# Kernel optimization log

Measured on AMD Instinct MI355X. Metric: run time of the kernel, lower is better.

The kernel has to match this reference:

```python
import jax, jax.numpy as jnp
import numpy as np

N, L, S, E, A, D = 16, 256, 128, 128, 9, 768
ARG_ROLES = 23      # score width = ARG_ROLES + 1
MAX_ARG = 9         # hard-coded max_len_arg in the torch module
N_HID = 768


def setup_inputs() -> dict:
    key = jax.random.key(0)
    ks = jax.random.split(key, 10)
    all_embeddings = jax.random.normal(ks[0], (N, L, D), jnp.float32)
    # last-3-layer BERT attention maps, 12 heads, positive entries
    attn_last3 = jax.random.uniform(ks[1], (3, N, 12, L, L), jnp.float32)
    # per-sample sorted distinct first-subword indices (all positive, full length:
    # the ragged filter idxs>0 then keeps everything -> fixed-shape gather)
    idx_keys = jax.random.split(ks[2], N)
    cand = jnp.arange(1, L - MAX_ARG - 1)
    idxs_to_collect = jax.vmap(
        lambda k: jnp.sort(jax.random.choice(k, cand, (S + 2,), replace=False))
    )(idx_keys).astype(jnp.int32)
    is_triggers = (jax.random.uniform(ks[3], (N, S)) < 0.05).astype(jnp.float32)
    is_triggers = is_triggers.at[:, 0].set(1.0)  # >=1 trigger per sample
    entity_mapping = jax.random.normal(ks[4], (N, S, E), jnp.float32) * 0.05
    arg_weight_matrices = jax.random.normal(ks[5], (N, MAX_ARG, A), jnp.float32) * 0.3
    map_keys = jax.random.split(ks[6], N)
    arg_mapping = jax.vmap(
        lambda k: jax.random.permutation(k, ARG_ROLES + 1)[:A]
    )(map_keys).astype(jnp.int32)
    W1 = jax.random.normal(ks[7], (6 * D, N_HID), jnp.float32) * 0.02
    b1 = jnp.zeros((N_HID,), jnp.float32)
    W2 = jax.random.normal(ks[8], (N_HID, 1), jnp.float32) * 0.02
    b2 = jnp.zeros((1,), jnp.float32)
    return {
        "all_embeddings": all_embeddings,
        "attn_last3": attn_last3,
        "entity_mapping": entity_mapping,
        "arg_weight_matrices": arg_weight_matrices,
        "is_triggers": is_triggers,
        "W1": W1, "b1": b1, "W2": W2, "b2": b2,
        "idxs_to_collect": idxs_to_collect,
        "arg_mapping": arg_mapping,
    }


def reference(all_embeddings, attn_last3, entity_mapping, arg_weight_matrices,
              is_triggers, W1, b1, W2, b2, idxs_to_collect, arg_mapping):
    sqrt_d = jnp.sqrt(jnp.asarray(D, jnp.float32))
    sent_idx = idxs_to_collect[:, :S]                      # [N,S] first-subword ids
    # get_fist_subword_embeddings: ragged gather (full-length here)
    sent_emb = jnp.take_along_axis(all_embeddings, sent_idx[:, :, None], axis=1)  # [N,S,D]
    # arg-type tokens sit right after the second-to-last [SEP]
    arg_pos = idxs_to_collect[:, -2:-1] + 1 + jnp.arange(MAX_ARG)[None, :]        # [N,9]
    arg_raw = jnp.take_along_axis(all_embeddings, arg_pos[:, :, None], axis=1)    # [N,9,D]

    entity_emb = jnp.einsum('nsd,nse->ned', sent_emb, entity_mapping)             # [N,E,D]
    trig = jnp.sum(sent_emb * is_triggers[..., None], axis=1) \
           / jnp.sum(is_triggers, axis=1, keepdims=True)                          # [N,D]
    del trig  # _trigger is computed but unused downstream in the torch forward
    arg_emb = jnp.einsum('nkd,nka->nad', arg_raw, arg_weight_matrices)            # [N,A,D]

    # bi-attention scores (broadcast-mul-sum == contraction over D)
    t2a = jnp.einsum('ned,nad->nea', entity_emb, arg_emb) / sqrt_d
    w = (t2a - 5.0) / 2.0                                                         # [N,E,A]
    token_argAwared = jnp.einsum('nea,nad->ned', w, arg_emb)                      # [N,E,D]
    arg_tokenAwared = jnp.einsum('nea,ned->nad', w, entity_emb)                   # [N,A,D]

    # select_hidden_att for each of the last 3 layers
    att_mean = jnp.mean(attn_last3, axis=2)                                       # [3,N,L,L]
    def sel_layer(a):  # a: [N,L,L] -> row/col gather + row renorm
        s = jax.vmap(lambda m, i: m[i][:, i])(a, sent_idx)                        # [N,S,S]
        return s / (jnp.sum(s, axis=-1, keepdims=True) + 1e-9)
    t2t = (sel_layer(att_mean[0]) + sel_layer(att_mean[1]) + sel_layer(att_mean[2])) / 3.0

    h2h_sent = jnp.einsum('nst,ntd->nsd', t2t, sent_emb)                          # [N,S,D]
    # A_h2h and H_ are projected from sent space (S) to entity space (E)
    A_h2h_e = jnp.einsum('nsd,nse->ned', h2h_sent, entity_mapping)                # [N,E,D]
    H_e = entity_emb                                                              # sent_emb projected == entity_emb

    a2a = jax.nn.softmax(jnp.einsum('nad,nbd->nab', arg_emb, arg_emb), axis=-1)   # [N,A,A]
    u2u = jnp.einsum('nab,nbd->nad', a2a, arg_emb)                                # [N,A,D]

    shp = (N, E, A, D)
    H_    = jnp.broadcast_to(H_e[:, :, None, :], shp)
    U_    = jnp.broadcast_to(arg_emb[:, None, :, :], shp)
    A_h2u = jnp.broadcast_to(token_argAwared[:, :, None, :], shp)
    A_h2h = jnp.broadcast_to(A_h2h_e[:, :, None, :], shp)
    A_u2h = jnp.broadcast_to(arg_tokenAwared[:, None, :, :], shp)
    A_u2u = jnp.broadcast_to(u2u[:, None, :, :], shp)
    latent = jnp.concatenate([H_, U_, A_h2u, A_h2h, A_u2h, A_u2u], axis=-1)       # [N,E,A,6D]

    hid = jax.nn.gelu(latent @ W1 + b1, approximate=False)                        # [N,E,A,768]
    score = (hid @ W2 + b2)[..., 0]                                               # [N,E,A]

    # map_arg_to_ids: scatter each arg slot back to its global role id
    def scatter_one(s, ids):  # s [E,A], ids [A]
        return jnp.full((E, ARG_ROLES + 1), -1e6, jnp.float32).at[:, ids].set(s)
    new_score = jax.vmap(scatter_one)(score, arg_mapping)                         # [N,E,24]
    return new_score
```

## Files before the change

### kernel.cpp

```cpp
#include <hip/hip_runtime.h>
#include <math.h>

namespace {
constexpr int N_ = 16, L_ = 256, S_ = 128, E_ = 128, A_ = 9, D_ = 768, H_ = 768, RO_ = 24;
constexpr int IDXW = 130;
constexpr int W1R = 6 * D_;
constexpr float INV_SQRT_D = 0.03608439182435161f;
constexpr int PESZ = 2048 * 768;
constexpr int PASZ = 144 * 768;
constexpr int GB_GATHER = 0;
constexpr int GB_ENTMAP = 192;
constexpr int GB_W1T    = 208;
constexpr int GB_T2T    = 1072;
constexpr int GB_ARGU   = 2096;
constexpr int GB_TOTAL  = 2112;
}

using bshort8 = __attribute__((ext_vector_type(8))) short;
using f32x4v = __attribute__((ext_vector_type(4))) float;

__device__ __forceinline__ unsigned short f2bf(float f) {
    unsigned u = __builtin_bit_cast(unsigned, f);
    return (unsigned short)((u + 0x7fffu + ((u >> 16) & 1u)) >> 16);
}

__global__ __launch_bounds__(256) void stage1_k(const float* __restrict__ all_emb,
                                                const int* __restrict__ idxs,
                                                const float* __restrict__ ent_map,
                                                const float* __restrict__ W1,
                                                const float* __restrict__ argw,
                                                const float* __restrict__ attn,
                                                unsigned short* __restrict__ sentT,
                                                unsigned short* __restrict__ entmapT,
                                                short* __restrict__ W1t,
                                                unsigned short* __restrict__ t2tbf,
                                                float* __restrict__ argE,
                                                unsigned short* __restrict__ argEbf,
                                                unsigned short* __restrict__ u2ubf) {
    __shared__ __align__(16) unsigned char smem[33792];
    const int b = blockIdx.x, tid = threadIdx.x;

    if (b < GB_ENTMAP) {
        const int n = b / 12, d0 = (b % 12) * 64;
        auto tile = (unsigned short (*)[132])smem;
#pragma unroll
        for (int it = 0; it < 8; ++it) {
            const int lin = tid + 256 * it;
            const int s = lin >> 4, dq = (lin & 15) * 4;
            const int row = idxs[n * IDXW + s];
            const float4 v = *reinterpret_cast<const float4*>(all_emb + ((size_t)(n * L_ + row)) * D_ + d0 + dq);
            tile[dq + 0][s] = f2bf(v.x); tile[dq + 1][s] = f2bf(v.y);
            tile[dq + 2][s] = f2bf(v.z); tile[dq + 3][s] = f2bf(v.w);
        }
        __syncthreads();
#pragma unroll
        for (int it = 0; it < 8; ++it) {
            const int lin = tid + 256 * it;
            const int d = lin >> 5, s4 = (lin & 31) * 4;
            ushort4 v = {tile[d][s4], tile[d][s4 + 1], tile[d][s4 + 2], tile[d][s4 + 3]};
            *reinterpret_cast<ushort4*>(sentT + ((size_t)(n * D_) + d0 + d) * S_ + s4) = v;
        }
    } else if (b < GB_W1T) {
        const int n = b - GB_ENTMAP;
        auto tile = (unsigned short (*)[132])smem;
#pragma unroll
        for (int it = 0; it < 16; ++it) {
            const int lin = tid + 256 * it;
            const int s = lin >> 5, eq = (lin & 31) * 4;
            const float4 v = *reinterpret_cast<const float4*>(ent_map + ((size_t)(n * S_ + s)) * E_ + eq);
            tile[eq + 0][s] = f2bf(v.x); tile[eq + 1][s] = f2bf(v.y);
            tile[eq + 2][s] = f2bf(v.z); tile[eq + 3][s] = f2bf(v.w);
        }
        __syncthreads();
#pragma unroll
        for (int it = 0; it < 16; ++it) {
            const int lin = tid + 256 * it;
            const int e = lin >> 5, s4 = (lin & 31) * 4;
            ushort4 v = {tile[e][s4], tile[e][s4 + 1], tile[e][s4 + 2], tile[e][s4 + 3]};
            *reinterpret_cast<ushort4*>(entmapT + ((size_t)(n * E_) + e) * S_ + s4) = v;
        }
    } else if (b < GB_T2T) {
        const int b2 = b - GB_W1T;
        const int k0 = (b2 % 72) * 64, h0 = (b2 / 72) * 64;
        auto tile = (float (*)[65])smem;
        const int tx = tid & 63, ty = tid >> 6;
#pragma unroll
        for (int i = 0; i < 16; ++i) {
            const int r = ty + i * 4;
            tile[r][tx] = W1[(size_t)(k0 + r) * H_ + h0 + tx];
        }
        __syncthreads();
#pragma unroll
        for (int i = 0; i < 16; ++i) {
            const int r = ty + i * 4;
            W1t[(size_t)(h0 + r) * W1R + k0 + tx] = (short)f2bf(tile[tx][r]);
        }
    } else if (b < GB_ARGU) {
        const int idx = b - GB_T2T;
        const int n = idx >> 6;
        const int half = tid >> 7, t128 = tid & 127;
        const int s = ((idx & 63) << 1) | half;
        const int w = t128 >> 6, lane = tid & 63;
        float* sum2 = (float*)smem;
        float* part = (float*)(smem + 12288);
        const int is = idxs[n * IDXW + s], it = idxs[n * IDXW + t128];
#pragma unroll
        for (int l = 0; l < 3; ++l) {
            const float* base = attn + ((size_t)((l * N_ + n) * 12 + w * 6)) * (L_ * L_)
                              + (size_t)is * L_ + lane * 4;
            float4 acc = {0.f, 0.f, 0.f, 0.f};
#pragma unroll
            for (int h = 0; h < 6; ++h) {
                const float4 v = *reinterpret_cast<const float4*>(base + (size_t)h * (L_ * L_));
                acc.x += v.x; acc.y += v.y; acc.z += v.z; acc.w += v.w;
            }
            *reinterpret_cast<float4*>(&sum2[(((half * 3 + l) * 2 + w) << 8) + lane * 4]) = acc;
        }
        __syncthreads();
        float m[3];
#pragma unroll
        for (int l = 0; l < 3; ++l) {
            m[l] = (sum2[(((half * 3 + l) * 2 + 0) << 8) + it] +
                    sum2[(((half * 3 + l) * 2 + 1) << 8) + it]) * (1.0f / 12.0f);
            float r = m[l];
#pragma unroll
            for (int off = 32; off; off >>= 1) r += __shfl_xor(r, off, 64);
            if (lane == 0) part[(half * 3 + l) * 2 + w] = r;
        }
        __syncthreads();
        float out = 0.f;
#pragma unroll
        for (int l = 0; l < 3; ++l)
            out += m[l] / (part[(half * 3 + l) * 2 + 0] + part[(half * 3 + l) * 2 + 1] + 1e-9f);
        t2tbf[((size_t)(n * S_ + s)) * S_ + t128] = f2bf(out * (1.0f / 3.0f));
    } else {
        const int n = b - GB_ARGU;
        auto wsm = (float (*)[A_])smem;
        auto part45 = (float (*)[4])(smem + 512);
        auto Psm = (float (*)[A_])(smem + 1536);
        if (tid < A_ * A_) wsm[tid / A_][tid % A_] = argw[n * A_ * A_ + tid];
        __syncthreads();
        const int p0 = idxs[n * IDXW + S_] + 1;
        float pp[45] = {};
        float vals[3][A_];
#pragma unroll
        for (int c = 0; c < 3; ++c) {
            const int d = tid + 256 * c;
            float raw[A_];
#pragma unroll
            for (int k = 0; k < A_; ++k) raw[k] = all_emb[((size_t)(n * L_ + p0 + k)) * D_ + d];
#pragma unroll
            for (int a = 0; a < A_; ++a) {
                float acc = 0.f;
#pragma unroll
                for (int k = 0; k < A_; ++k) acc = fmaf(raw[k], wsm[k][a], acc);
                vals[c][a] = acc;
                argE[((size_t)(n * A_ + a)) * D_ + d] = acc;
                argEbf[((size_t)(n * A_ + a)) * D_ + d] = f2bf(acc);
            }
            int p = 0;
#pragma unroll
            for (int a = 0; a < A_; ++a)
#pragma unroll
                for (int bb = a; bb < A_; ++bb) pp[p++] += vals[c][a] * vals[c][bb];
        }
        const int lane = tid & 63, wv = tid >> 6;
#pragma unroll
        for (int p = 0; p < 45; ++p) {
            float v = pp[p];
            for (int off = 32; off; off >>= 1) v += __shfl_down(v, off, 64);
            if (lane == 0) part45[p][wv] = v;
        }
        __syncthreads();
        if (tid < 45) part45[tid][0] = part45[tid][0] + part45[tid][1] + part45[tid][2] + part45[tid][3];
        __syncthreads();
        if (tid < A_) {
            const int a = tid;
            float v[A_], mx = -1e30f;
#pragma unroll
            for (int bb = 0; bb < A_; ++bb) {
                const int lo = a < bb ? a : bb, hi = a < bb ? bb : a;
                v[bb] = part45[lo * (19 - lo) / 2 + hi - lo][0];
                mx = fmaxf(mx, v[bb]);
            }
            float sm = 0.f;
#pragma unroll
            for (int bb = 0; bb < A_; ++bb) { v[bb] = expf(v[bb] - mx); sm += v[bb]; }
            const float inv = 1.0f / sm;
#pragma unroll
            for (int bb = 0; bb < A_; ++bb) Psm[a][bb] = v[bb] * inv;
        }
        __syncthreads();
#pragma unroll
        for (int c = 0; c < 3; ++c) {
            const int d = tid + 256 * c;
#pragma unroll
            for (int a = 0; a < A_; ++a) {
                float acc = 0.f;
#pragma unroll
                for (int bb = 0; bb < A_; ++bb) acc = fmaf(Psm[a][bb], vals[c][bb], acc);
                u2ubf[((size_t)(n * A_ + a)) * D_ + d] = f2bf(acc);
            }
        }
    }
}

__global__ __launch_bounds__(256) void gemm_pair_k(const unsigned short* __restrict__ t2tbf,
                                                   const unsigned short* __restrict__ entmapT,
                                                   const unsigned short* __restrict__ sentT,
                                                   float* __restrict__ entf,
                                                   unsigned short* __restrict__ entbf,
                                                   unsigned short* __restrict__ h2hT) {
    __shared__ __align__(16) short As[128][40];
    __shared__ __align__(16) short Bs[64][40];
    const int n = blockIdx.y, c0 = blockIdx.x * 64, z = blockIdx.z;
    const unsigned short* A = (z == 0 ? t2tbf : entmapT) + (size_t)n * S_ * S_;
    const unsigned short* BT = sentT + (size_t)n * D_ * S_;
    const int tid = threadIdx.x;
    const int wave = tid >> 6, lane = tid & 63;
    const int row16 = lane & 15, quad = lane >> 4;
    f32x4v acc[2][4] = {};
    for (int k0 = 0; k0 < S_; k0 += 32) {
#pragma unroll
        for (int i = 0; i < 2; ++i) {
            const int idx = tid + 256 * i;
            const int r = idx >> 2, q = idx & 3;
            *reinterpret_cast<bshort8*>(&As[r][q * 8]) =
                *reinterpret_cast<const bshort8*>(A + (size_t)r * S_ + k0 + q * 8);
        }
        {
            const int col = tid >> 2, q = tid & 3;
            *reinterpret_cast<bshort8*>(&Bs[col][q * 8]) =
                *reinterpret_cast<const bshort8*>(BT + (size_t)(c0 + col) * S_ + k0 + q * 8);
        }
        __syncthreads();
        bshort8 a[2], b[4];
#pragma unroll
        for (int mi = 0; mi < 2; ++mi)
            a[mi] = *reinterpret_cast<const bshort8*>(&As[wave * 32 + mi * 16 + row16][quad * 8]);
#pragma unroll
        for (int ni = 0; ni < 4; ++ni)
            b[ni] = *reinterpret_cast<const bshort8*>(&Bs[ni * 16 + row16][quad * 8]);
#pragma unroll
        for (int mi = 0; mi < 2; ++mi)
#pragma unroll
            for (int ni = 0; ni < 4; ++ni)
                acc[mi][ni] = __builtin_amdgcn_mfma_f32_16x16x32_bf16(a[mi], b[ni], acc[mi][ni], 0, 0, 0);
        __syncthreads();
    }
#pragma unroll
    for (int mi = 0; mi < 2; ++mi) {
#pragma unroll
        for (int ni = 0; ni < 4; ++ni) {
            const int rbase = wave * 32 + mi * 16 + quad * 4;
            const int col = c0 + ni * 16 + row16;
            if (z == 0) {
                ushort4 v = {f2bf(acc[mi][ni][0]), f2bf(acc[mi][ni][1]),
                             f2bf(acc[mi][ni][2]), f2bf(acc[mi][ni][3])};
                *reinterpret_cast<ushort4*>(h2hT + (size_t)n * D_ * S_ + (size_t)col * S_ + rbase) = v;
            } else {
#pragma unroll
                for (int t = 0; t < 4; ++t) {
                    const size_t o = ((size_t)n * S_ + rbase + t) * D_ + col;
                    entf[o] = acc[mi][ni][t];
                    entbf[o] = f2bf(acc[mi][ni][t]);
                }
            }
        }
    }
}

__global__ __launch_bounds__(256) void gemm2_k(const unsigned short* __restrict__ entmapT,
                                               const unsigned short* __restrict__ h2hT,
                                               const unsigned short* __restrict__ entbf,
                                               const unsigned short* __restrict__ argEbf,
                                               unsigned short* __restrict__ Ah2hbf,
                                               float* __restrict__ wbuf) {
    const int bx = blockIdx.x, tid = threadIdx.x;
    const int wave = tid >> 6, lane = tid & 63;
    const int row16 = lane & 15, quad = lane >> 4;
    if (bx < 192) {
        __shared__ __align__(16) short As[128][40];
        __shared__ __align__(16) short Bs[64][40];
        const int n = bx / 12, c0 = (bx % 12) * 64;
        const unsigned short* A = entmapT + (size_t)n * S_ * S_;
        const unsigned short* BT = h2hT + (size_t)n * D_ * S_;
        f32x4v acc[2][4] = {};
        for (int k0 = 0; k0 < S_; k0 += 32) {
#pragma unroll
            for (int i = 0; i < 2; ++i) {
                const int idx = tid + 256 * i;
                const int r = idx >> 2, q = idx & 3;
                *reinterpret_cast<bshort8*>(&As[r][q * 8]) =
                    *reinterpret_cast<const bshort8*>(A + (size_t)r * S_ + k0 + q * 8);
            }
            {
                const int col = tid >> 2, q = tid & 3;
                *reinterpret_cast<bshort8*>(&Bs[col][q * 8]) =
                    *reinterpret_cast<const bshort8*>(BT + (size_t)(c0 + col) * S_ + k0 + q * 8);
            }
            __syncthreads();
            bshort8 a[2], b[4];
#pragma unroll
            for (int mi = 0; mi < 2; ++mi)
                a[mi] = *reinterpret_cast<const bshort8*>(&As[wave * 32 + mi * 16 + row16][quad * 8]);
#pragma unroll
            for (int ni = 0; ni < 4; ++ni)
                b[ni] = *reinterpret_cast<const bshort8*>(&Bs[ni * 16 + row16][quad * 8]);
#pragma unroll
            for (int mi = 0; mi < 2; ++mi)
#pragma unroll
                for (int ni = 0; ni < 4; ++ni)
                    acc[mi][ni] = __builtin_amdgcn_mfma_f32_16x16x32_bf16(a[mi], b[ni], acc[mi][ni], 0, 0, 0);
            __syncthreads();
        }
#pragma unroll
        for (int mi = 0; mi < 2; ++mi)
#pragma unroll
            for (int ni = 0; ni < 4; ++ni) {
                const int rbase = wave * 32 + mi * 16 + quad * 4;
                const int col = c0 + ni * 16 + row16;
#pragma unroll
                for (int t = 0; t < 4; ++t)
                    Ah2hbf[((size_t)n * S_ + rbase + t) * D_ + col] = f2bf(acc[mi][ni][t]);
            }
    } else {
        const int n = bx - 192;
        const unsigned short* Aent = entbf + (size_t)n * E_ * D_;
        const unsigned short* Barg = argEbf + (size_t)n * A_ * D_;
        f32x4v acc[2] = {};
        for (int k0 = 0; k0 < D_; k0 += 32) {
            bshort8 a[2], b;
#pragma unroll
            for (int mi = 0; mi < 2; ++mi)
                a[mi] = *reinterpret_cast<const bshort8*>(Aent + (size_t)(wave * 32 + mi * 16 + row16) * D_ + k0 + quad * 8);
            b = *reinterpret_cast<const bshort8*>(Barg + (size_t)row16 * D_ + k0 + quad * 8);
#pragma unroll
            for (int mi = 0; mi < 2; ++mi)
                acc[mi] = __builtin_amdgcn_mfma_f32_16x16x32_bf16(a[mi], b, acc[mi], 0, 0, 0);
        }
        if (row16 < A_) {
#pragma unroll
            for (int mi = 0; mi < 2; ++mi)
#pragma unroll
                for (int t = 0; t < 4; ++t) {
                    const int e = wave * 32 + mi * 16 + quad * 4 + t;
                    const float w = (acc[mi][t] * INV_SQRT_D - 5.0f) * 0.5f;
                    wbuf[((size_t)(n * E_ + e)) * A_ + row16] = w;
                }
        }
    }
}

__global__ __launch_bounds__(256) void post_k(const float* __restrict__ wbuf,
                                              const float* __restrict__ argE,
                                              const float* __restrict__ entf,
                                              unsigned short* __restrict__ tokAbf,
                                              unsigned short* __restrict__ argTbf) {
    const int b = blockIdx.x, tid = threadIdx.x;
    if (b < N_ * E_) {
        const int n = b >> 7, e = b & 127;
        __shared__ float wl[A_];
        if (tid < A_) wl[tid] = wbuf[(size_t)(n * E_ + e) * A_ + tid];
        __syncthreads();
        const float* ar = argE + (size_t)n * A_ * D_;
#pragma unroll
        for (int c = 0; c < 3; ++c) {
            const int d = tid + 256 * c;
            float s = 0.f;
#pragma unroll
            for (int a = 0; a < A_; ++a) s = fmaf(wl[a], ar[(size_t)a * D_ + d], s);
            tokAbf[((size_t)(n * E_ + e)) * D_ + d] = f2bf(s);
        }
    } else {
        const int idx = b - N_ * E_;
        const int n = idx / A_, a = idx % A_;
        __shared__ float wl[E_];
        if (tid < E_) wl[tid] = wbuf[(size_t)(n * E_ + tid) * A_ + a];
        __syncthreads();
        const float* eb = entf + (size_t)n * E_ * D_;
#pragma unroll
        for (int c = 0; c < 3; ++c) {
            const int d = tid + 256 * c;
            float acc = 0.f;
            for (int e = 0; e < E_; ++e) acc = fmaf(wl[e], eb[(size_t)e * D_ + d], acc);
            argTbf[((size_t)(n * A_ + a)) * D_ + d] = f2bf(acc);
        }
    }
}

__global__ __launch_bounds__(256) void mfma_mlp_k(const unsigned short* __restrict__ e0,
                                                  const unsigned short* __restrict__ e1,
                                                  const unsigned short* __restrict__ e2,
                                                  const unsigned short* __restrict__ a0,
                                                  const unsigned short* __restrict__ a1,
                                                  const unsigned short* __restrict__ a2,
                                                  const short* __restrict__ W1t,
                                                  float* __restrict__ Pe3, float* __restrict__ Pa3) {
    __shared__ __align__(16) short As[128][40];
    __shared__ __align__(16) short Bs[64][40];
    const int bx = blockIdx.x;
    const int seg = bx % 3;
    const int blk = bx / 3;
    const bool isPa = blk >= 16;
    const unsigned short* Aseg;
    int woff;
    if (isPa) {
        Aseg = seg == 0 ? a0 : (seg == 1 ? a1 : a2);
        woff = seg == 0 ? 1 * D_ : (seg == 1 ? 4 * D_ : 5 * D_);
    } else {
        Aseg = seg == 0 ? e0 : (seg == 1 ? e1 : e2);
        woff = seg == 0 ? 0 : (seg == 1 ? 2 * D_ : 3 * D_);
    }
    const int M = isPa ? N_ * A_ : N_ * E_;
    const int r0 = (isPa ? blk - 16 : blk) * 128;
    float* C = isPa ? (Pa3 + (size_t)seg * PASZ) : (Pe3 + (size_t)seg * PESZ);
    const int c0 = blockIdx.y * 64;
    const int tid = threadIdx.x;
    const int wave = tid >> 6, lane = tid & 63;
    const int row16 = lane & 15, quad = lane >> 4;
    f32x4v acc[2][4] = {};
    for (int kk = 0; kk < D_; kk += 32) {
#pragma unroll
        for (int i = 0; i < 2; ++i) {
            const int idx = tid + 256 * i;
            const int r = idx >> 2, q = idx & 3;
            bshort8 av = {};
            if (r0 + r < M) av = *reinterpret_cast<const bshort8*>(Aseg + (size_t)(r0 + r) * D_ + kk + q * 8);
            *reinterpret_cast<bshort8*>(&As[r][q * 8]) = av;
        }
        {
            const int col = tid >> 2, q = tid & 3;
            *reinterpret_cast<bshort8*>(&Bs[col][q * 8]) =
                *reinterpret_cast<const bshort8*>(W1t + (size_t)(c0 + col) * W1R + woff + kk + q * 8);
        }
        __syncthreads();
        bshort8 a[2], b[4];
#pragma unroll
        for (int mi = 0; mi < 2; ++mi)
            a[mi] = *reinterpret_cast<const bshort8*>(&As[wave * 32 + mi * 16 + row16][quad * 8]);
#pragma unroll
        for (int ni = 0; ni < 4; ++ni)
            b[ni] = *reinterpret_cast<const bshort8*>(&Bs[ni * 16 + row16][quad * 8]);
#pragma unroll
        for (int mi = 0; mi < 2; ++mi)
#pragma unroll
            for (int ni = 0; ni < 4; ++ni)
                acc[mi][ni] = __builtin_amdgcn_mfma_f32_16x16x32_bf16(a[mi], b[ni], acc[mi][ni], 0, 0, 0);
        __syncthreads();
    }
#pragma unroll
    for (int mi = 0; mi < 2; ++mi) {
#pragma unroll
        for (int ni = 0; ni < 4; ++ni) {
            const int rbase = r0 + wave * 32 + mi * 16 + quad * 4;
            const int col = c0 + ni * 16 + row16;
#pragma unroll
            for (int t = 0; t < 4; ++t)
                if (rbase + t < M) C[(size_t)(rbase + t) * H_ + col] = acc[mi][ni][t];
        }
    }
}

__global__ __launch_bounds__(256) void score_k(const float* __restrict__ Pe3, const float* __restrict__ Pa3,
                                               const float* __restrict__ b1, const float* __restrict__ W2,
                                               const float* __restrict__ b2, const int* __restrict__ arg_map,
                                               float* __restrict__ out) {
    const int n = blockIdx.x >> 7, e = blockIdx.x & 127;
    const int tid = threadIdx.x;
    __shared__ float paS[A_ * H_];
    __shared__ float part[A_][4];
    float* orow = out + ((size_t)(n * E_ + e)) * RO_;
    if (tid < RO_) orow[tid] = -1000000.0f;
    for (int i = tid; i < A_ * H_; i += 256) {
        const size_t o = (size_t)n * A_ * H_ + i;
        paS[i] = Pa3[o] + Pa3[PASZ + o] + Pa3[2 * PASZ + o];
    }
    __syncthreads();
    const size_t ro = ((size_t)(n * E_ + e)) * H_;
    float acc[A_] = {};
    for (int h = tid; h < H_; h += 256) {
        const float pe = Pe3[ro + h] + Pe3[PESZ + ro + h] + Pe3[2 * PESZ + ro + h] + b1[h];
        const float w2 = W2[h];
#pragma unroll
        for (int a = 0; a < A_; ++a) {
            const float x = pe + paS[a * H_ + h];
            const float g = x * 0.5f * (1.0f + erff(x * 0.70710678118654752f));
            acc[a] = fmaf(g, w2, acc[a]);
        }
    }
    const int lane = tid & 63, wv = tid >> 6;
#pragma unroll
    for (int a = 0; a < A_; ++a)
        for (int off = 32; off; off >>= 1) acc[a] += __shfl_down(acc[a], off, 64);
    if (lane == 0)
        for (int a = 0; a < A_; ++a) part[a][wv] = acc[a];
    __syncthreads();
    if (tid < A_) {
        const float s = part[tid][0] + part[tid][1] + part[tid][2] + part[tid][3] + b2[0];
        orow[arg_map[n * A_ + tid]] = s;
    }
}

extern "C" void kernel_launch(void* const* d_in, const int* in_sizes, int n_in,
                              void* d_out, int out_size, void* d_ws, size_t ws_size,
                              hipStream_t stream) {
    const float* all_emb = (const float*)d_in[0];
    const float* attn    = (const float*)d_in[1];
    const float* ent_map = (const float*)d_in[2];
    const float* argw    = (const float*)d_in[3];
    const float* W1 = (const float*)d_in[5];
    const float* b1 = (const float*)d_in[6];
    const float* W2 = (const float*)d_in[7];
    const float* b2 = (const float*)d_in[8];
    const int* idxs    = (const int*)d_in[9];
    const int* arg_map = (const int*)d_in[10];
    float* out = (float*)d_out;

    float* ws = (float*)d_ws;
    float* entf = ws + 0;
    float* Pe3  = ws + 1572864;
    float* argE = ws + 6291456;
    float* wbuf = ws + 6402048;
    float* Pa3  = ws + 6420480;
    short*          W1t     = (short*)(ws + 6752256);
    unsigned short* sentT   = (unsigned short*)(ws + 8521728);
    unsigned short* entmapT = (unsigned short*)(ws + 9308160);
    unsigned short* t2tbf   = (unsigned short*)(ws + 9439232);
    unsigned short* argEbf  = (unsigned short*)(ws + 9570304);
    unsigned short* u2ubf   = (unsigned short*)(ws + 9625600);
    unsigned short* entbf   = (unsigned short*)(ws + 9680896);
    unsigned short* h2hT    = (unsigned short*)(ws + 10467328);
    unsigned short* Ah2hbf  = (unsigned short*)(ws + 11253760);
    unsigned short* tokAbf  = (unsigned short*)(ws + 12040192);
    unsigned short* argTbf  = (unsigned short*)(ws + 12826624);

    stage1_k<<<GB_TOTAL, 256, 0, stream>>>(all_emb, idxs, ent_map, W1, argw, attn,
                                           sentT, entmapT, W1t, t2tbf, argE, argEbf, u2ubf);

    gemm_pair_k<<<dim3(D_ / 64, N_, 2), 256, 0, stream>>>(t2tbf, entmapT, sentT, entf, entbf, h2hT);

    gemm2_k<<<208, 256, 0, stream>>>(entmapT, h2hT, entbf, argEbf, Ah2hbf, wbuf);

    post_k<<<N_ * E_ + N_ * A_, 256, 0, stream>>>(wbuf, argE, entf, tokAbf, argTbf);

    mfma_mlp_k<<<dim3(54, H_ / 64), 256, 0, stream>>>(entbf, tokAbf, Ah2hbf, argEbf, argTbf, u2ubf, W1t, Pe3, Pa3);

    score_k<<<N_ * E_, 256, 0, stream>>>(Pe3, Pa3, b1, W2, b2, arg_map, out);

    (void)in_sizes; (void)n_in; (void)out_size; (void)ws_size;
}
```

Before: 318.2 us.

## Reassociate A_h2h chain via entmap·t2t product and fuse post-GEMM stages

Instead of computing h2h = t2t·sent and then entmap·h2h over D columns, the code first forms the small S×S product entmap·t2t and then multiplies it by the sentence embeddings. This cuts the 768-wide intermediate GEMM. The gemm2/post kernels are merged into a single fused kernel that also computes the entity-arg weights in place with fp32 dot products, which drops one launch and the wbuf round-trip. It also reorders stage1 block ranges so the heavy t2t blocks go first, and swaps the MLP grid axes so column tiles vary fastest. The reassociation changes bf16 rounding order, and the fp32 dot-product loops may be slower per block.

Result: slower. 329.7 us (+3.6%).

```diff
diff --git a/kernel.cpp b/kernel.cpp
--- a/kernel.cpp
+++ b/kernel.cpp
@@ -8,10 +8,10 @@
 constexpr float INV_SQRT_D = 0.03608439182435161f;
 constexpr int PESZ = 2048 * 768;
 constexpr int PASZ = 144 * 768;
-constexpr int GB_GATHER = 0;
-constexpr int GB_ENTMAP = 192;
-constexpr int GB_W1T    = 208;
-constexpr int GB_T2T    = 1072;
+constexpr int GB_T2T    = 0;
+constexpr int GB_W1T    = 1024;
+constexpr int GB_GATHER = 1888;
+constexpr int GB_ENTMAP = 2080;
 constexpr int GB_ARGU   = 2096;
 constexpr int GB_TOTAL  = 2112;
 }
@@ -22,6 +22,43 @@
 __device__ __forceinline__ unsigned short f2bf(float f) {
     unsigned u = __builtin_bit_cast(unsigned, f);
     return (unsigned short)((u + 0x7fffu + ((u >> 16) & 1u)) >> 16);
+}
+
+__device__ __forceinline__ void gemm_body128(const unsigned short* __restrict__ A,
+                                             const unsigned short* __restrict__ BT,
+                                             int lda, int ldb, int c0, int tid,
+                                             short (*As)[40], short (*Bs)[40],
+                                             f32x4v acc[2][4]) {
+    const int wave = tid >> 6, lane = tid & 63;
+    const int row16 = lane & 15, quad = lane >> 4;
+    for (int k0 = 0; k0 < S_; k0 += 32) {
+#pragma unroll
+        for (int i = 0; i < 2; ++i) {
+            const int idx = tid + 256 * i;
+            const int r = idx >> 2, q = idx & 3;
+            *reinterpret_cast<bshort8*>(&As[r][q * 8]) =
+                *reinterpret_cast<const bshort8*>(A + (size_t)r * lda + k0 + q * 8);
+        }
+        {
+            const int col = tid >> 2, q = tid & 3;
+            *reinterpret_cast<bshort8*>(&Bs[col][q * 8]) =
+                *reinterpret_cast<const bshort8*>(BT + (size_t)(c0 + col) * ldb + k0 + q * 8);
+        }
+        __syncthreads();
+        bshort8 a[2], b[4];
+#pragma unroll
+        for (int mi = 0; mi < 2; ++mi)
+            a[mi] = *reinterpret_cast<const bshort8*>(&As[wave * 32 + mi * 16 + row16][quad * 8]);
+#pragma unroll
+        for (int ni = 0; ni < 4; ++ni)
+            b[ni] = *reinterpret_cast<const bshort8*>(&Bs[ni * 16 + row16][quad * 8]);
+#pragma unroll
+        for (int mi = 0; mi < 2; ++mi)
+#pragma unroll
+            for (int ni = 0; ni < 4; ++ni)
+                acc[mi][ni] = __builtin_amdgcn_mfma_f32_16x16x32_bf16(a[mi], b[ni], acc[mi][ni], 0, 0, 0);
+        __syncthreads();
+    }
 }
 
 __global__ __launch_bounds__(256) void stage1_k(const float* __restrict__ all_emb,
@@ -33,15 +70,77 @@
                                                 unsigned short* __restrict__ sentT,
                                                 unsigned short* __restrict__ entmapT,
                                                 short* __restrict__ W1t,
-                                                unsigned short* __restrict__ t2tbf,
+                                                unsigned short* __restrict__ t2tT,
                                                 float* __restrict__ argE,
                                                 unsigned short* __restrict__ argEbf,
                                                 unsigned short* __restrict__ u2ubf) {
     __shared__ __align__(16) unsigned char smem[33792];
     const int b = blockIdx.x, tid = threadIdx.x;
 
-    if (b < GB_ENTMAP) {
-        const int n = b / 12, d0 = (b % 12) * 64;
+    if (b < GB_W1T) {
+        const int idx = b - GB_T2T;
+        const int n = idx >> 6;
+        const int half = tid >> 7, t128 = tid & 127;
+        const int s0 = (idx & 63) << 1;
+        const int s = s0 | half;
+        const int w = t128 >> 6, lane = tid & 63;
+        float* sum2 = (float*)smem;
+        float* part = (float*)(smem + 12288);
+        unsigned short* tileT = (unsigned short*)(smem + 12544);
+        const int is = idxs[n * IDXW + s], it = idxs[n * IDXW + t128];
+#pragma unroll
+        for (int l = 0; l < 3; ++l) {
+            const float* base = attn + ((size_t)((l * N_ + n) * 12 + w * 6)) * (L_ * L_)
+                              + (size_t)is * L_ + lane * 4;
+            float4 acc = {0.f, 0.f, 0.f, 0.f};
+#pragma unroll
+            for (int h = 0; h < 6; ++h) {
+                const float4 v = *reinterpret_cast<const float4*>(base + (size_t)h * (L_ * L_));
+                acc.x += v.x; acc.y += v.y; acc.z += v.z; acc.w += v.w;
+            }
+            *reinterpret_cast<float4*>(&sum2[(((half * 3 + l) * 2 + w) << 8) + lane * 4]) = acc;
+        }
+        __syncthreads();
+        float m[3];
+#pragma unroll
+        for (int l = 0; l < 3; ++l) {
+            m[l] = (sum2[(((half * 3 + l) * 2 + 0) << 8) + it] +
+                    sum2[(((half * 3 + l) * 2 + 1) << 8) + it]) * (1.0f / 12.0f);
+            float r = m[l];
+#pragma unroll
+            for (int off = 32; off; off >>= 1) r += __shfl_xor(r, off, 64);
+            if (lane == 0) part[(half * 3 + l) * 2 + w] = r;
+        }
+        __syncthreads();
+        float out = 0.f;
+#pragma unroll
+        for (int l = 0; l < 3; ++l)
+            out += m[l] / (part[(half * 3 + l) * 2 + 0] + part[(half * 3 + l) * 2 + 1] + 1e-9f);
+        tileT[t128 * 2 + half] = f2bf(out * (1.0f / 3.0f));
+        __syncthreads();
+        if (tid < 128) {
+            const unsigned int v = ((const unsigned int*)tileT)[tid];
+            *reinterpret_cast<unsigned int*>(t2tT + ((size_t)(n * S_) + tid) * S_ + s0) = v;
+        }
+    } else if (b < GB_GATHER) {
+        const int b2 = b - GB_W1T;
+        const int k0 = (b2 % 72) * 64, h0 = (b2 / 72) * 64;
+        auto tile = (float (*)[65])smem;
+        const int tx = tid & 63, ty = tid >> 6;
+#pragma unroll
+        for (int i = 0; i < 16; ++i) {
+            const int r = ty + i * 4;
+            tile[r][tx] = W1[(size_t)(k0 + r) * H_ + h0 + tx];
+        }
+        __syncthreads();
+#pragma unroll
+        for (int i = 0; i < 16; ++i) {
+            const int r = ty + i * 4;
+            W1t[(size_t)(h0 + r) * W1R + k0 + tx] = (short)f2bf(tile[tx][r]);
+        }
+    } else if (b < GB_ENTMAP) {
+        const int b2 = b - GB_GATHER;
+        const int n = b2 / 12, d0 = (b2 % 12) * 64;
         auto tile = (unsigned short (*)[132])smem;
 #pragma unroll
         for (int it = 0; it < 8; ++it) {
@@ -60,7 +159,7 @@
             ushort4 v = {tile[d][s4], tile[d][s4 + 1], tile[d][s4 + 2], tile[d][s4 + 3]};
             *reinterpret_cast<ushort4*>(sentT + ((size_t)(n * D_) + d0 + d) * S_ + s4) = v;
         }
-    } else if (b < GB_W1T) {
+    } else if (b < GB_ARGU) {
         const int n = b - GB_ENTMAP;
         auto tile = (unsigned short (*)[132])smem;
 #pragma unroll
@@ -79,60 +178,6 @@
             ushort4 v = {tile[e][s4], tile[e][s4 + 1], tile[e][s4 + 2], tile[e][s4 + 3]};
             *reinterpret_cast<ushort4*>(entmapT + ((size_t)(n * E_) + e) * S_ + s4) = v;
         }
-    } else if (b < GB_T2T) {
-        const int b2 = b - GB_W1T;
-        const int k0 = (b2 % 72) * 64, h0 = (b2 / 72) * 64;
-        auto tile = (float (*)[65])smem;
-        const int tx = tid & 63, ty = tid >> 6;
-#pragma unroll
-        for (int i = 0; i < 16; ++i) {
-            const int r = ty + i * 4;
-            tile[r][tx] = W1[(size_t)(k0 + r) * H_ + h0 + tx];
-        }
-        __syncthreads();
-#pragma unroll
-        for (int i = 0; i < 16; ++i) {
-            const int r = ty + i * 4;
-            W1t[(size_t)(h0 + r) * W1R + k0 + tx] = (short)f2bf(tile[tx][r]);
-        }
-    } else if (b < GB_ARGU) {
-        const int idx = b - GB_T2T;
-        const int n = idx >> 6;
-        const int half = tid >> 7, t128 = tid & 127;
-        const int s = ((idx & 63) << 1) | half;
-        const int w = t128 >> 6, lane = tid & 63;
-        float* sum2 = (float*)smem;
-        float* part = (float*)(smem + 12288);
-        const int is = idxs[n * IDXW + s], it = idxs[n * IDXW + t128];
-#pragma unroll
-        for (int l = 0; l < 3; ++l) {
-            const float* base = attn + ((size_t)((l * N_ + n) * 12 + w * 6)) * (L_ * L_)
-                              + (size_t)is * L_ + lane * 4;
-            float4 acc = {0.f, 0.f, 0.f, 0.f};
-#pragma unroll
-            for (int h = 0; h < 6; ++h) {
-                const float4 v = *reinterpret_cast<const float4*>(base + (size_t)h * (L_ * L_));
-                acc.x += v.x; acc.y += v.y; acc.z += v.z; acc.w += v.w;
-            }
-            *reinterpret_cast<float4*>(&sum2[(((half * 3 + l) * 2 + w) << 8) + lane * 4]) = acc;
-        }
-        __syncthreads();
-        float m[3];
-#pragma unroll
-        for (int l = 0; l < 3; ++l) {
-            m[l] = (sum2[(((half * 3 + l) * 2 + 0) << 8) + it] +
-                    sum2[(((half * 3 + l) * 2 + 1) << 8) + it]) * (1.0f / 12.0f);
-            float r = m[l];
-#pragma unroll
-            for (int off = 32; off; off >>= 1) r += __shfl_xor(r, off, 64);
-            if (lane == 0) part[(half * 3 + l) * 2 + w] = r;
-        }
-        __syncthreads();
-        float out = 0.f;
-#pragma unroll
-        for (int l = 0; l < 3; ++l)
-            out += m[l] / (part[(half * 3 + l) * 2 + 0] + part[(half * 3 + l) * 2 + 1] + 1e-9f);
-        t2tbf[((size_t)(n * S_ + s)) * S_ + t128] = f2bf(out * (1.0f / 3.0f));
     } else {
         const int n = b - GB_ARGU;
         auto wsm = (float (*)[A_])smem;
@@ -205,115 +250,40 @@
     }
 }
 
-__global__ __launch_bounds__(256) void gemm_pair_k(const unsigned short* __restrict__ t2tbf,
-                                                   const unsigned short* __restrict__ entmapT,
-                                                   const unsigned short* __restrict__ sentT,
-                                                   float* __restrict__ entf,
-                                                   unsigned short* __restrict__ entbf,
-                                                   unsigned short* __restrict__ h2hT) {
+__global__ __launch_bounds__(256) void gemm_entM1_k(const unsigned short* __restrict__ entmapT,
+                                                    const unsigned short* __restrict__ sentT,
+                                                    const unsigned short* __restrict__ t2tT,
+                                                    float* __restrict__ entf,
+                                                    unsigned short* __restrict__ entbf,
+                                                    unsigned short* __restrict__ M1bf) {
     __shared__ __align__(16) short As[128][40];
     __shared__ __align__(16) short Bs[64][40];
-    const int n = blockIdx.y, c0 = blockIdx.x * 64, z = blockIdx.z;
-    const unsigned short* A = (z == 0 ? t2tbf : entmapT) + (size_t)n * S_ * S_;
-    const unsigned short* BT = sentT + (size_t)n * D_ * S_;
-    const int tid = threadIdx.x;
+    const int bx = blockIdx.x, tid = threadIdx.x;
     const int wave = tid >> 6, lane = tid & 63;
     const int row16 = lane & 15, quad = lane >> 4;
     f32x4v acc[2][4] = {};
-    for (int k0 = 0; k0 < S_; k0 += 32) {
-#pragma unroll
-        for (int i = 0; i < 2; ++i) {
-            const int idx = tid + 256 * i;
-            const int r = idx >> 2, q = idx & 3;
-            *reinterpret_cast<bshort8*>(&As[r][q * 8]) =
-                *reinterpret_cast<const bshort8*>(A + (size_t)r * S_ + k0 + q * 8);
-        }
-        {
-            const int col = tid >> 2, q = tid & 3;
-            *reinterpret_cast<bshort8*>(&Bs[col][q * 8]) =
-                *reinterpret_cast<const bshort8*>(BT + (size_t)(c0 + col) * S_ + k0 + q * 8);
-        }
-        __syncthreads();
-        bshort8 a[2], b[4];
-#pragma unroll
-        for (int mi = 0; mi < 2; ++mi)
-            a[mi] = *reinterpret_cast<const bshort8*>(&As[wave * 32 + mi * 16 + row16][quad * 8]);
-#pragma unroll
-        for (int ni = 0; ni < 4; ++ni)
-            b[ni] = *reinterpret_cast<const bshort8*>(&Bs[ni * 16 + row16][quad * 8]);
-#pragma unroll
-        for (int mi = 0; mi < 2; ++mi)
-#pragma unroll
-            for (int ni = 0; ni < 4; ++ni)
-                acc[mi][ni] = __builtin_amdgcn_mfma_f32_16x16x32_bf16(a[mi], b[ni], acc[mi][ni], 0, 0, 0);
-        __syncthreads();
-    }
-#pragma unroll
-    for (int mi = 0; mi < 2; ++mi) {
-#pragma unroll
-        for (int ni = 0; ni < 4; ++ni) {
-            const int rbase = wave * 32 + mi * 16 + quad * 4;
-            const int col = c0 + ni * 16 + row16;
-            if (z == 0) {
-                ushort4 v = {f2bf(acc[mi][ni][0]), f2bf(acc[mi][ni][1]),
-                             f2bf(acc[mi][ni][2]), f2bf(acc[mi][ni][3])};
-                *reinterpret_cast<ushort4*>(h2hT + (size_t)n * D_ * S_ + (size_t)col * S_ + rbase) = v;
-            } else {
+    if (bx < 192) {
+        const int n = bx / 12, c0 = (bx % 12) * 64;
+        gemm_body128(entmapT + (size_t)n * S_ * S_, sentT + (size_t)n * D_ * S_,
+                     S_, S_, c0, tid, As, Bs, acc);
+#pragma unroll
+        for (int mi = 0; mi < 2; ++mi)
+#pragma unroll
+            for (int ni = 0; ni < 4; ++ni) {
+                const int rbase = wave * 32 + mi * 16 + quad * 4;
+                const int col = c0 + ni * 16 + row16;
 #pragma unroll
                 for (int t = 0; t < 4; ++t) {
-                    const size_t o = ((size_t)n * S_ + rbase + t) * D_ + col;
+                    const size_t o = ((size_t)(n * S_) + rbase + t) * D_ + col;
                     entf[o] = acc[mi][ni][t];
                     entbf[o] = f2bf(acc[mi][ni][t]);
                 }
             }
-        }
-    }
-}
-
-__global__ __launch_bounds__(256) void gemm2_k(const unsigned short* __restrict__ entmapT,
-                                               const unsigned short* __restrict__ h2hT,
-                                               const unsigned short* __restrict__ entbf,
-                                               const unsigned short* __restrict__ argEbf,
-                                               unsigned short* __restrict__ Ah2hbf,
-                                               float* __restrict__ wbuf) {
-    const int bx = blockIdx.x, tid = threadIdx.x;
-    const int wave = tid >> 6, lane = tid & 63;
-    const int row16 = lane & 15, quad = lane >> 4;
-    if (bx < 192) {
-        __shared__ __align__(16) short As[128][40];
-        __shared__ __align__(16) short Bs[64][40];
-        const int n = bx / 12, c0 = (bx % 12) * 64;
-        const unsigned short* A = entmapT + (size_t)n * S_ * S_;
-        const unsigned short* BT = h2hT + (size_t)n * D_ * S_;
-        f32x4v acc[2][4] = {};
-        for (int k0 = 0; k0 < S_; k0 += 32) {
-#pragma unroll
-            for (int i = 0; i < 2; ++i) {
-                const int idx = tid + 256 * i;
-                const int r = idx >> 2, q = idx & 3;
-                *reinterpret_cast<bshort8*>(&As[r][q * 8]) =
-                    *reinterpret_cast<const bshort8*>(A + (size_t)r * S_ + k0 + q * 8);
-            }
-            {
-                const int col = tid >> 2, q = tid & 3;
-                *reinterpret_cast<bshort8*>(&Bs[col][q * 8]) =
-                    *reinterpret_cast<const bshort8*>(BT + (size_t)(c0 + col) * S_ + k0 + q * 8);
-            }
-            __syncthreads();
-            bshort8 a[2], b[4];
-#pragma unroll
-            for (int mi = 0; mi < 2; ++mi)
-                a[mi] = *reinterpret_cast<const bshort8*>(&As[wave * 32 + mi * 16 + row16][quad * 8]);
-#pragma unroll
-            for (int ni = 0; ni < 4; ++ni)
-                b[ni] = *reinterpret_cast<const bshort8*>(&Bs[ni * 16 + row16][quad * 8]);
-#pragma unroll
-            for (int mi = 0; mi < 2; ++mi)
-#pragma unroll
-                for (int ni = 0; ni < 4; ++ni)
-                    acc[mi][ni] = __builtin_amdgcn_mfma_f32_16x16x32_bf16(a[mi], b[ni], acc[mi][ni], 0, 0, 0);
-            __syncthreads();
-        }
+    } else {
+        const int idx = bx - 192;
+        const int n = idx >> 1, c0 = (idx & 1) * 64;
+        gemm_body128(entmapT + (size_t)n * S_ * S_, t2tT + (size_t)n * S_ * S_,
+                     S_, S_, c0, tid, As, Bs, acc);
 #pragma unroll
         for (int mi = 0; mi < 2; ++mi)
 #pragma unroll
@@ -322,61 +292,34 @@
                 const int col = c0 + ni * 16 + row16;
 #pragma unroll
                 for (int t = 0; t < 4; ++t)
-                    Ah2hbf[((size_t)n * S_ + rbase + t) * D_ + col] = f2bf(acc[mi][ni][t]);
-            }
-    } else {
-        const int n = bx - 192;
-        const unsigned short* Aent = entbf + (size_t)n * E_ * D_;
-        const unsigned short* Barg = argEbf + (size_t)n * A_ * D_;
-        f32x4v acc[2] = {};
-        for (int k0 = 0; k0 < D_; k0 += 32) {
-            bshort8 a[2], b;
-#pragma unroll
-            for (int mi = 0; mi < 2; ++mi)
-                a[mi] = *reinterpret_cast<const bshort8*>(Aent + (size_t)(wave * 32 + mi * 16 + row16) * D_ + k0 + quad * 8);
-            b = *reinterpret_cast<const bshort8*>(Barg + (size_t)row16 * D_ + k0 + quad * 8);
-#pragma unroll
-            for (int mi = 0; mi < 2; ++mi)
-                acc[mi] = __builtin_amdgcn_mfma_f32_16x16x32_bf16(a[mi], b, acc[mi], 0, 0, 0);
-        }
-        if (row16 < A_) {
-#pragma unroll
-            for (int mi = 0; mi < 2; ++mi)
-#pragma unroll
-                for (int t = 0; t < 4; ++t) {
-                    const int e = wave * 32 + mi * 16 + quad * 4 + t;
-                    const float w = (acc[mi][t] * INV_SQRT_D - 5.0f) * 0.5f;
-                    wbuf[((size_t)(n * E_ + e)) * A_ + row16] = w;
-                }
-        }
-    }
-}
-
-__global__ __launch_bounds__(256) void post_k(const float* __restrict__ wbuf,
-                                              const float* __restrict__ argE,
-                                              const float* __restrict__ entf,
-                                              unsigned short* __restrict__ tokAbf,
-                                              unsigned short* __restrict__ argTbf) {
-    const int b = blockIdx.x, tid = threadIdx.x;
-    if (b < N_ * E_) {
-        const int n = b >> 7, e = b & 127;
-        __shared__ float wl[A_];
-        if (tid < A_) wl[tid] = wbuf[(size_t)(n * E_ + e) * A_ + tid];
-        __syncthreads();
-        const float* ar = argE + (size_t)n * A_ * D_;
-#pragma unroll
-        for (int c = 0; c < 3; ++c) {
-            const int d = tid + 256 * c;
-            float s = 0.f;
-#pragma unroll
-            for (int a = 0; a < A_; ++a) s = fmaf(wl[a], ar[(size_t)a * D_ + d], s);
-            tokAbf[((size_t)(n * E_ + e)) * D_ + d] = f2bf(s);
-        }
-    } else {
-        const int idx = b - N_ * E_;
-        const int n = idx / A_, a = idx % A_;
-        __shared__ float wl[E_];
-        if (tid < E_) wl[tid] = wbuf[(size_t)(n * E_ + tid) * A_ + a];
+                    M1bf[((size_t)(n * S_) + rbase + t) * S_ + col] = f2bf(acc[mi][ni][t]);
+            }
+    }
+}
+
+__global__ __launch_bounds__(256) void fused3_k(const unsigned short* __restrict__ M1bf,
+                                                const unsigned short* __restrict__ sentT,
+                                                const float* __restrict__ entf,
+                                                const float* __restrict__ argE,
+                                                unsigned short* __restrict__ Ah2hbf,
+                                                unsigned short* __restrict__ tokAbf,
+                                                unsigned short* __restrict__ argTbf) {
+    __shared__ __align__(16) unsigned char smem[15872];
+    const int bx = blockIdx.x, tid = threadIdx.x;
+    if (bx < N_ * A_) {
+        const int n = bx / A_, a = bx % A_;
+        float* argS = (float*)smem;
+        float* wl = (float*)(smem + 3072);
+        for (int i = tid; i < D_; i += 256) argS[i] = argE[((size_t)(n * A_ + a)) * D_ + i];
+        __syncthreads();
+        {
+            const int e = tid >> 1, h = tid & 1;
+            const float* er = entf + ((size_t)(n * E_ + e)) * D_ + h * 384;
+            float p = 0.f;
+            for (int d = 0; d < 384; ++d) p = fmaf(er[d], argS[h * 384 + d], p);
+            p += __shfl_down(p, 1, 64);
+            if (h == 0) wl[e] = (p * INV_SQRT_D - 5.0f) * 0.5f;
+        }
         __syncthreads();
         const float* eb = entf + (size_t)n * E_ * D_;
 #pragma unroll
@@ -385,6 +328,58 @@
             float acc = 0.f;
             for (int e = 0; e < E_; ++e) acc = fmaf(wl[e], eb[(size_t)e * D_ + d], acc);
             argTbf[((size_t)(n * A_ + a)) * D_ + d] = f2bf(acc);
+        }
+    } else if (bx < N_ * A_ + 192) {
+        const int idx = bx - N_ * A_;
+        const int n = idx / 12, c0 = (idx % 12) * 64;
+        short (*As)[40] = (short (*)[40])smem;
+        short (*Bs)[40] = (short (*)[40])(smem + 10240);
+        const int wave = tid >> 6, lane = tid & 63;
+        const int row16 = lane & 15, quad = lane >> 4;
+        f32x4v acc[2][4] = {};
+        gemm_body128(M1bf + (size_t)n * S_ * S_, sentT + (size_t)n * D_ * S_,
+                     S_, S_, c0, tid, As, Bs, acc);
+#pragma unroll
+        for (int mi = 0; mi < 2; ++mi)
+#pragma unroll
+            for (int ni = 0; ni < 4; ++ni) {
+                const int rbase = wave * 32 + mi * 16 + quad * 4;
+                const int col = c0 + ni * 16 + row16;
+#pragma unroll
+                for (int t = 0; t < 4; ++t)
+                    Ah2hbf[((size_t)(n * S_) + rbase + t) * D_ + col] = f2bf(acc[mi][ni][t]);
+            }
+    } else {
+        const int idx = bx - (N_ * A_ + 192);
+        const int n = idx >> 7, e = idx & 127;
+        float* wl = (float*)smem;
+        float* part = (float*)(smem + 64);
+        const float* er = entf + ((size_t)(n * E_ + e)) * D_;
+        const float* ar = argE + (size_t)n * A_ * D_;
+        float acc[A_] = {};
+        for (int d = tid; d < D_; d += 256) {
+            const float ev = er[d];
+#pragma unroll
+            for (int a = 0; a < A_; ++a) acc[a] = fmaf(ev, ar[(size_t)a * D_ + d], acc[a]);
+        }
+        const int lane = tid & 63, wv = tid >> 6;
+#pragma unroll
+        for (int a = 0; a < A_; ++a)
+            for (int off = 32; off; off >>= 1) acc[a] += __shfl_down(acc[a], off, 64);
+        if (lane == 0)
+            for (int a = 0; a < A_; ++a) part[a * 4 + wv] = acc[a];
+        __syncthreads();
+        if (tid < A_)
+            wl[tid] = ((part[tid * 4] + part[tid * 4 + 1] + part[tid * 4 + 2] + part[tid * 4 + 3])
+                       * INV_SQRT_D - 5.0f) * 0.5f;
+        __syncthreads();
+#pragma unroll
+        for (int c = 0; c < 3; ++c) {
+            const int d = tid + 256 * c;
+            float s = 0.f;
+#pragma unroll
+            for (int a = 0; a < A_; ++a) s = fmaf(wl[a], ar[(size_t)a * D_ + d], s);
+            tokAbf[((size_t)(n * E_ + e)) * D_ + d] = f2bf(s);
         }
     }
 }
@@ -399,9 +394,10 @@
                                                   float* __restrict__ Pe3, float* __restrict__ Pa3) {
     __shared__ __align__(16) short As[128][40];
     __shared__ __align__(16) short Bs[64][40];
-    const int bx = blockIdx.x;
-    const int seg = bx % 3;
-    const int blk = bx / 3;
+    const int c0 = blockIdx.x * 64;
+    const int by = blockIdx.y;
+    const int seg = by / 18;
+    const int blk = by % 18;
     const bool isPa = blk >= 16;
     const unsigned short* Aseg;
     int woff;
@@ -415,7 +411,6 @@
     const int M = isPa ? N_ * A_ : N_ * E_;
     const int r0 = (isPa ? blk - 16 : blk) * 128;
     float* C = isPa ? (Pa3 + (size_t)seg * PASZ) : (Pe3 + (size_t)seg * PESZ);
-    const int c0 = blockIdx.y * 64;
     const int tid = threadIdx.x;
     const int wave = tid >> 6, lane = tid & 63;
     const int row16 = lane & 15, quad = lane >> 4;
@@ -521,30 +516,28 @@
     float* entf = ws + 0;
     float* Pe3  = ws + 1572864;
     float* argE = ws + 6291456;
-    float* wbuf = ws + 6402048;
-    float* Pa3  = ws + 6420480;
-    short*          W1t     = (short*)(ws + 6752256);
-    unsigned short* sentT   = (unsigned short*)(ws + 8521728);
-    unsigned short* entmapT = (unsigned short*)(ws + 9308160);
-    unsigned short* t2tbf   = (unsigned short*)(ws + 9439232);
-    unsigned short* argEbf  = (unsigned short*)(ws + 9570304);
-    unsigned short* u2ubf   = (unsigned short*)(ws + 9625600);
-    unsigned short* entbf   = (unsigned short*)(ws + 9680896);
-    unsigned short* h2hT    = (unsigned short*)(ws + 10467328);
-    unsigned short* Ah2hbf  = (unsigned short*)(ws + 11253760);
-    unsigned short* tokAbf  = (unsigned short*)(ws + 12040192);
-    unsigned short* argTbf  = (unsigned short*)(ws + 12826624);
+    float* Pa3  = ws + 6402048;
+    short*          W1t     = (short*)(ws + 6733824);
+    unsigned short* sentT   = (unsigned short*)(ws + 8503296);
+    unsigned short* entmapT = (unsigned short*)(ws + 9289728);
+    unsigned short* t2tT    = (unsigned short*)(ws + 9420800);
+    unsigned short* M1bf    = (unsigned short*)(ws + 9551872);
+    unsigned short* argEbf  = (unsigned short*)(ws + 9682944);
+    unsigned short* u2ubf   = (unsigned short*)(ws + 9738240);
+    unsigned short* entbf   = (unsigned short*)(ws + 9793536);
+    unsigned short* Ah2hbf  = (unsigned short*)(ws + 10579968);
+    unsigned short* tokAbf  = (unsigned short*)(ws + 11366400);
+    unsigned short* argTbf  = (unsigned short*)(ws + 12152832);
 
     stage1_k<<<GB_TOTAL, 256, 0, stream>>>(all_emb, idxs, ent_map, W1, argw, attn,
-                                           sentT, entmapT, W1t, t2tbf, argE, argEbf, u2ubf);
-
-    gemm_pair_k<<<dim3(D_ / 64, N_, 2), 256, 0, stream>>>(t2tbf, entmapT, sentT, entf, entbf, h2hT);
-
-    gemm2_k<<<208, 256, 0, stream>>>(entmapT, h2hT, entbf, argEbf, Ah2hbf, wbuf);
-
-    post_k<<<N_ * E_ + N_ * A_, 256, 0, stream>>>(wbuf, argE, entf, tokAbf, argTbf);
-
-    mfma_mlp_k<<<dim3(54, H_ / 64), 256, 0, stream>>>(entbf, tokAbf, Ah2hbf, argEbf, argTbf, u2ubf, W1t, Pe3, Pa3);
+                                           sentT, entmapT, W1t, t2tT, argE, argEbf, u2ubf);
+
+    gemm_entM1_k<<<224, 256, 0, stream>>>(entmapT, sentT, t2tT, entf, entbf, M1bf);
+
+    fused3_k<<<N_ * A_ + 192 + N_ * E_, 256, 0, stream>>>(M1bf, sentT, entf, argE,
+                                                          Ah2hbf, tokAbf, argTbf);
+
+    mfma_mlp_k<<<dim3(12, 54), 256, 0, stream>>>(entbf, tokAbf, Ah2hbf, argEbf, argTbf, u2ubf, W1t, Pe3, Pa3);
 
     score_k<<<N_ * E_, 256, 0, stream>>>(Pe3, Pa3, b1, W2, b2, arg_map, out);
 
```
